# Optimization experiments

Measured on AMD Instinct MI355X. Metric: run time of the kernel, lower is better.

The kernel has to match this reference:

```python
import jax, jax.numpy as jnp
import numpy as np

GRAVITY = 9.81007  # pypose default, gravity vector [0,0,g]

# Quaternions are xyzw (pypose SO3 convention). q1*q2 composes rotations R1@R2.

def qmul(q1, q2):
    v1, w1 = q1[..., :3], q1[..., 3:]
    v2, w2 = q2[..., :3], q2[..., 3:]
    w = w1 * w2 - jnp.sum(v1 * v2, axis=-1, keepdims=True)
    v = w1 * v2 + w2 * v1 + jnp.cross(v1, v2)
    return jnp.concatenate([v, w], axis=-1)

def qinv(q):
    return jnp.concatenate([-q[..., :3], q[..., 3:]], axis=-1)

def qrot(q, v):
    # rotate vector v by unit quaternion q: v + 2*cross(qv, cross(qv,v) + qw*v)
    qv, qw = q[..., :3], q[..., 3:]
    t = jnp.cross(qv, v) + qw * v
    return v + 2.0 * jnp.cross(qv, t)

def so3_exp(phi):
    # so3 -> SO3 quaternion: q = [phi*sin(|phi|/2)/|phi|, cos(|phi|/2)]
    theta = jnp.linalg.norm(phi, axis=-1, keepdims=True)
    small = theta < 1e-6
    safe = jnp.where(small, 1.0, theta)
    k = jnp.where(small, 0.5 - theta * theta / 48.0, jnp.sin(0.5 * theta) / safe)
    return jnp.concatenate([phi * k, jnp.cos(0.5 * theta)], axis=-1)


def setup_inputs() -> dict:
    key = jax.random.key(0)
    ks = jax.random.split(key, 7)
    B, F = 64, 32768
    dt = jax.random.uniform(ks[0], (B, F, 1), jnp.float32) * 0.01 + 0.004
    gyro = jax.random.normal(ks[1], (B, F, 3), jnp.float32) * 0.1
    acc = jax.random.normal(ks[2], (B, F, 3), jnp.float32)

    def rand_quat(k, shape):
        q = jax.random.normal(k, shape + (4,), jnp.float32)
        return q / jnp.linalg.norm(q, axis=-1, keepdims=True)

    gt_rot = rand_quat(ks[3], (B, F))      # ground-truth orientations (xyzw)
    init_rot = rand_quat(ks[4], (B, 1))
    init_vel = jax.random.normal(ks[5], (B, 1, 3), jnp.float32)
    init_pos = jax.random.normal(ks[6], (B, 1, 3), jnp.float32)
    return dict(dt=dt, gyro=gyro, acc=acc, gt_rot=gt_rot,
                init_rot=init_rot, init_vel=init_vel, init_pos=init_pos)


def reference(dt, gyro, acc, gt_rot, init_rot, init_vel, init_pos):
    # IMU preintegration (pypose IMUPreintegrator, reset=True, prop_cov=False,
    # training branch: gravity removed in body frame via ground-truth rot).
    g = jnp.array([0.0, 0.0, GRAVITY], dtype=dt.dtype)
    dr = so3_exp(gyro * dt)                                   # (B,F,4) per-step rotation
    # cumulative rotation increment: incre_r[i] = dr_0 * dr_1 * ... * dr_i
    incre_r = jax.lax.associative_scan(qmul, dr, axis=1)      # (B,F,4)
    # gravity-compensated body-frame acceleration
    a = acc - qrot(qinv(gt_rot), g)                           # (B,F,3)
    ra = qrot(incre_r, a)                                     # rotated into init frame
    incre_v = jnp.cumsum(ra * dt, axis=1)                     # (B,F,3)
    v_prev = jnp.concatenate([jnp.zeros_like(incre_v[:, :1]), incre_v[:, :-1]], axis=1)
    incre_p = jnp.cumsum(v_prev * dt + 0.5 * ra * dt * dt, axis=1)
    incre_t = jnp.cumsum(dt, axis=1)                          # (B,F,1)
    # compose with initial state
    rot = qmul(init_rot, incre_r)                             # (B,F,4)
    vel = init_vel + qrot(init_rot, incre_v)                  # (B,F,3)
    pos = init_pos + init_vel * incre_t + qrot(init_rot, incre_p)  # (B,F,3)
    return rot, vel, pos
```

## Files before the change

### kernel.cpp

```cpp
#include <hip/hip_runtime.h>
#include <math.h>

namespace {

constexpr int SEQ    = 4;
constexpr int WCHUNK = 64 * SEQ;

constexpr int GY_F  = 0;
constexpr int AC_F  = 768;
constexpr int GT_F  = 1536;
constexpr int BUF_F = 2560;

struct V3 { float x, y, z; };
struct Q4 { float x, y, z, w; };
struct St { Q4 q; V3 s; V3 p; float T; float pad; };

__device__ __forceinline__ Q4 qmul(const Q4 a, const Q4 b) {
  Q4 r;
  r.x = a.w*b.x + b.w*a.x + a.y*b.z - a.z*b.y;
  r.y = a.w*b.y + b.w*a.y + a.z*b.x - a.x*b.z;
  r.z = a.w*b.z + b.w*a.z + a.x*b.y - a.y*b.x;
  r.w = a.w*b.w - a.x*b.x - a.y*b.y - a.z*b.z;
  return r;
}

__device__ __forceinline__ V3 qrot(const Q4 q, const V3 v) {
  float tx = q.y*v.z - q.z*v.y + q.w*v.x;
  float ty = q.z*v.x - q.x*v.z + q.w*v.y;
  float tz = q.x*v.y - q.y*v.x + q.w*v.z;
  V3 r;
  r.x = v.x + 2.0f*(q.y*tz - q.z*ty);
  r.y = v.y + 2.0f*(q.z*tx - q.x*tz);
  r.z = v.z + 2.0f*(q.x*ty - q.y*tx);
  return r;
}

__device__ __forceinline__ St combine(const St a, const St b) {
  St r;
  r.q = qmul(a.q, b.q);
  V3 rs = qrot(a.q, b.s);
  r.s.x = a.s.x + rs.x;
  r.s.y = a.s.y + rs.y;
  r.s.z = a.s.z + rs.z;
  V3 rp = qrot(a.q, b.p);
  r.p.x = a.p.x + a.s.x*b.T + rp.x;
  r.p.y = a.p.y + a.s.y*b.T + rp.y;
  r.p.z = a.p.z + a.s.z*b.T + rp.z;
  r.T = a.T + b.T;
  r.pad = 0.0f;
  return r;
}

__device__ __forceinline__ St identity_st() {
  St r;
  r.q = {0.0f, 0.0f, 0.0f, 1.0f};
  r.s = {0.0f, 0.0f, 0.0f};
  r.p = {0.0f, 0.0f, 0.0f};
  r.T = 0.0f; r.pad = 0.0f;
  return r;
}

struct El { Q4 q; V3 s; float dt; };

__device__ __forceinline__ El elem_state(float dt, V3 w, V3 ac, Q4 gt) {
  float px = w.x*dt, py = w.y*dt, pz = w.z*dt;
  float t2 = px*px + py*py + pz*pz;
  float k  = 0.5f + t2*(-1.0f/48.0f  + t2*(1.0f/3840.0f));
  float cw = 1.0f + t2*(-0.125f      + t2*(1.0f/384.0f));
  Q4 dr = { px*k, py*k, pz*k, cw };
  Q4 gi = { -gt.x, -gt.y, -gt.z, gt.w };
  V3 g  = { 0.0f, 0.0f, 9.81007f };
  V3 gr = qrot(gi, g);
  V3 a  = { ac.x - gr.x, ac.y - gr.y, ac.z - gr.z };
  V3 ra = qrot(dr, a);
  El e;
  e.q = dr;
  e.s = { ra.x*dt, ra.y*dt, ra.z*dt };
  e.dt = dt;
  return e;
}

__device__ __forceinline__ Q4 shfl_up_q(const Q4 v, int d) {
  return { __shfl_up(v.x,d), __shfl_up(v.y,d), __shfl_up(v.z,d), __shfl_up(v.w,d) };
}
__device__ __forceinline__ V3 shfl_up_v(const V3 v, int d) {
  return { __shfl_up(v.x,d), __shfl_up(v.y,d), __shfl_up(v.z,d) };
}

__device__ __forceinline__ St shfl_up_st(const St& v, int d) {
  St r;
  r.q.x = __shfl_up(v.q.x, d); r.q.y = __shfl_up(v.q.y, d);
  r.q.z = __shfl_up(v.q.z, d); r.q.w = __shfl_up(v.q.w, d);
  r.s.x = __shfl_up(v.s.x, d); r.s.y = __shfl_up(v.s.y, d);
  r.s.z = __shfl_up(v.s.z, d);
  r.p.x = __shfl_up(v.p.x, d); r.p.y = __shfl_up(v.p.y, d);
  r.p.z = __shfl_up(v.p.z, d);
  r.T   = __shfl_up(v.T, d);   r.pad = 0.0f;
  return r;
}

__device__ __forceinline__ St bcast_st(const St& v, int src) {
  St r;
  r.q.x = __shfl(v.q.x, src); r.q.y = __shfl(v.q.y, src);
  r.q.z = __shfl(v.q.z, src); r.q.w = __shfl(v.q.w, src);
  r.s.x = __shfl(v.s.x, src); r.s.y = __shfl(v.s.y, src);
  r.s.z = __shfl(v.s.z, src);
  r.p.x = __shfl(v.p.x, src); r.p.y = __shfl(v.p.y, src);
  r.p.z = __shfl(v.p.z, src);
  r.T   = __shfl(v.T, src);   r.pad = 0.0f;
  return r;
}

__device__ __forceinline__ int swz(int byteoff) {
  return byteoff ^ (((byteoff >> 8) & 3) << 4);
}
__device__ __forceinline__ float4& L4(float* lds, int fidx) {
  return *reinterpret_cast<float4*>(reinterpret_cast<char*>(lds) + swz(fidx << 2));
}

__device__ __forceinline__ void stage16(const void* gsrc, void* ldst) {
  __builtin_amdgcn_global_load_lds(
      (const __attribute__((address_space(1))) void*)gsrc,
      (__attribute__((address_space(3))) void*)ldst, 16, 0, 0);
}

#define STAGE_REGION(gbase, bufByte, nK)                                       \
  {                                                                            \
    _Pragma("unroll")                                                          \
    for (int k = 0; k < (nK); ++k) {                                           \
      int db = k*1024 + t*16;                                                  \
      const char* src = (const char*)(gbase) + swz(db);                        \
      char* ldst = (char*)lds + (bufByte) + k*1024;                            \
      stage16(src, ldst);                                                      \
    }                                                                          \
  }

struct Compressed { float cq[12]; float cs[12]; float cdt[4]; };
struct Seg { Q4 q; V3 s; V3 p; float T; };
struct ScanRes { Q4 qex, qin; V3 sex, sin; V3 pex, pin; float Tex, Tin; };

__device__ __forceinline__ Seg build_slim(float* lds, int ofs, int t,
                                          float4 dt4, Compressed& C) {
  float gy[12], ac[12], gq[16];
  #pragma unroll
  for (int j = 0; j < 3; ++j) ((float4*)gy)[j] = L4(lds, ofs + GY_F + 12*t + 4*j);
  #pragma unroll
  for (int j = 0; j < 3; ++j) ((float4*)ac)[j] = L4(lds, ofs + AC_F + 12*t + 4*j);
  #pragma unroll
  for (int j = 0; j < 4; ++j) ((float4*)gq)[j] = L4(lds, ofs + GT_F + 16*t + 4*j);
  const float dtv[4] = {dt4.x, dt4.y, dt4.z, dt4.w};
  Seg s;
  #pragma unroll
  for (int i = 0; i < SEQ; ++i) {
    El e = elem_state(dtv[i],
               {gy[3*i], gy[3*i+1], gy[3*i+2]},
               {ac[3*i], ac[3*i+1], ac[3*i+2]},
               {gq[4*i], gq[4*i+1], gq[4*i+2], gq[4*i+3]});
    C.cq[3*i] = e.q.x; C.cq[3*i+1] = e.q.y; C.cq[3*i+2] = e.q.z;
    C.cs[3*i] = e.s.x; C.cs[3*i+1] = e.s.y; C.cs[3*i+2] = e.s.z;
    C.cdt[i]  = e.dt;
    if (i == 0) {
      s.q = e.q; s.s = e.s;
      float h = 0.5f*e.dt;
      s.p = { e.s.x*h, e.s.y*h, e.s.z*h };
      s.T = e.dt;
    } else {
      V3 v = qrot(s.q, e.s);
      float h = 0.5f*e.dt;
      s.p.x += s.s.x*e.dt + v.x*h;
      s.p.y += s.s.y*e.dt + v.y*h;
      s.p.z += s.s.z*e.dt + v.z*h;
      s.s.x += v.x; s.s.y += v.y; s.s.z += v.z;
      s.q = qmul(s.q, e.q);
      s.T += e.dt;
    }
  }
  return s;
}

__device__ __forceinline__ ScanRes wave_split_scan(int t, const Seg& sg) {
  ScanRes r;
  Q4 qin = sg.q;
  #pragma unroll
  for (int d = 1; d < 64; d <<= 1) {
    Q4 o = shfl_up_q(qin, d);
    if (t >= d) qin = qmul(o, qin);
  }
  Q4 qex = shfl_up_q(qin, 1);
  if (t == 0) qex = {0.0f, 0.0f, 0.0f, 1.0f};
  V3 v = qrot(qex, sg.s);
  V3 sin_ = v;
  #pragma unroll
  for (int d = 1; d < 64; d <<= 1) {
    V3 o = shfl_up_v(sin_, d);
    if (t >= d) { sin_.x += o.x; sin_.y += o.y; sin_.z += o.z; }
  }
  V3 sex = shfl_up_v(sin_, 1);
  if (t == 0) sex = {0.0f, 0.0f, 0.0f};
  float Tin = sg.T;
  #pragma unroll
  for (int d = 1; d < 64; d <<= 1) {
    float o = __shfl_up(Tin, d);
    if (t >= d) Tin += o;
  }
  float Tex = __shfl_up(Tin, 1);
  if (t == 0) Tex = 0.0f;
  V3 w = qrot(qex, sg.p);
  V3 u = { w.x + sex.x*sg.T, w.y + sex.y*sg.T, w.z + sex.z*sg.T };
  V3 pin = u;
  #pragma unroll
  for (int d = 1; d < 64; d <<= 1) {
    V3 o = shfl_up_v(pin, d);
    if (t >= d) { pin.x += o.x; pin.y += o.y; pin.z += o.z; }
  }
  V3 pex = shfl_up_v(pin, 1);
  if (t == 0) pex = {0.0f, 0.0f, 0.0f};
  r.qex = qex; r.qin = qin;
  r.sex = sex; r.sin = sin_;
  r.pex = pex; r.pin = pin;
  r.Tex = Tex; r.Tin = Tin;
  return r;
}

__device__ __forceinline__ void compute_outputs(
    const Compressed& C, Q4 Pq, V3 Ps, V3 Pp, float PT,
    const ScanRes& S, V3 iv, V3 ip,
    float* rotb , float* velb , float* posb )
{
  Q4 Xq = qmul(Pq, S.qex);
  V3 rs = qrot(Pq, S.sex);
  V3 Xs = { Ps.x + rs.x, Ps.y + rs.y, Ps.z + rs.z };
  V3 rp = qrot(Pq, S.pex);
  V3 Xp = { Pp.x + Ps.x*S.Tex + rp.x, Pp.y + Ps.y*S.Tex + rp.y,
            Pp.z + Ps.z*S.Tex + rp.z };
  float XT = PT + S.Tex;

  Q4 qr = Xq; V3 sr = Xs; V3 pr = Xp; float Tr = XT;
  #pragma unroll
  for (int i = 0; i < SEQ; ++i) {
    float qx = C.cq[3*i], qy = C.cq[3*i+1], qz = C.cq[3*i+2];
    Q4 eq = { qx, qy, qz, sqrtf(fmaxf(1.0f - qx*qx - qy*qy - qz*qz, 0.0f)) };
    V3 es = { C.cs[3*i], C.cs[3*i+1], C.cs[3*i+2] };
    float dt = C.cdt[i], h = 0.5f*dt;
    V3 vv = qrot(qr, es);
    V3 pn = { pr.x + sr.x*dt + vv.x*h,
              pr.y + sr.y*dt + vv.y*h,
              pr.z + sr.z*dt + vv.z*h };
    V3 sn = { sr.x + vv.x, sr.y + vv.y, sr.z + vv.z };
    Q4 qn = qmul(qr, eq);
    float Tn = Tr + dt;
    rotb[4*i+0] = qn.x; rotb[4*i+1] = qn.y; rotb[4*i+2] = qn.z; rotb[4*i+3] = qn.w;
    velb[3*i+0] = iv.x + sn.x;
    velb[3*i+1] = iv.y + sn.y;
    velb[3*i+2] = iv.z + sn.z;
    posb[3*i+0] = ip.x + iv.x*Tn + pn.x;
    posb[3*i+1] = ip.y + iv.y*Tn + pn.y;
    posb[3*i+2] = ip.z + iv.z*Tn + pn.z;
    qr = qn; sr = sn; pr = pn; Tr = Tn;
  }
}

__global__ __launch_bounds__(64) void k_agg(
    const float* __restrict__ dtp, const float* __restrict__ gyp,
    const float* __restrict__ acp, const float* __restrict__ gtp,
    St* __restrict__ aggs)
{
  __shared__ __align__(16) float lds[BUF_F];
  const int t = threadIdx.x;
  const size_t base = (size_t)blockIdx.x * WCHUNK;

  STAGE_REGION(gyp + base*3, 0,    3);
  STAGE_REGION(acp + base*3, 3072, 3);
  STAGE_REGION(gtp + base*4, 6144, 4);
  float4 dt4 = ((const float4*)(dtp + base))[t];
  __syncthreads();

  Compressed C;
  Seg s = build_slim(lds, 0, t, dt4, C);
  ScanRes R = wave_split_scan(t, s);

  if (t == 63) {
    St a;
    a.q = R.qin; a.s = R.sin; a.p = R.pin; a.T = R.Tin; a.pad = 0.0f;
    aggs[blockIdx.x] = a;
  }
}

__global__ __launch_bounds__(64) void k_pref(
    const St* __restrict__ aggs, const float* __restrict__ irp,
    float* __restrict__ prefb, int cpb)
{
  const int b = blockIdx.x;
  const int lane = threadIdx.x & 63;

  St carry = identity_st();
  carry.q = { irp[b*4+0], irp[b*4+1], irp[b*4+2], irp[b*4+3] };

  const int nw = (cpb + 63) >> 6;
  for (int w = 0; w < nw; ++w) {
    const int idx = (w << 6) + lane;
    St A = identity_st();
    if (idx < cpb) A = aggs[(size_t)b*cpb + idx];
    #pragma unroll
    for (int d = 1; d < 64; d <<= 1) {
      St o = shfl_up_st(A, d);
      if (lane >= d) A = combine(o, A);
    }
    St ex = shfl_up_st(A, 1);
    St P = (lane == 0) ? carry : combine(carry, ex);
    if (idx < cpb) {
      float4* pp = (float4*)(prefb + ((size_t)b*cpb + idx)*12);
      pp[0] = make_float4(P.q.x, P.q.y, P.q.z, P.q.w);
      pp[1] = make_float4(P.s.x, P.s.y, P.s.z, P.p.x);
      pp[2] = make_float4(P.p.y, P.p.z, P.T, 0.0f);
    }
    carry = combine(carry, bcast_st(A, 63));
  }
}

__global__ __launch_bounds__(64) void k_emit(
    const float* __restrict__ dtp, const float* __restrict__ gyp,
    const float* __restrict__ acp, const float* __restrict__ gtp,
    const float* __restrict__ prefb,
    const float* __restrict__ ivp, const float* __restrict__ ipp,
    float* __restrict__ out, int F, int cpb, int B)
{
  __shared__ __align__(16) float lds[2*BUF_F];
  const int t = threadIdx.x;
  const int cid0 = blockIdx.x*2, cid1 = cid0 + 1;
  const int b0 = cid0 / cpb, b1 = cid1 / cpb;
  const size_t base0 = (size_t)cid0 * WCHUNK;
  const size_t base1 = (size_t)cid1 * WCHUNK;

  Q4 Pq0, Pq1; V3 Ps0, Pp0, Ps1, Pp1; float PT0, PT1;
  {
    const float4* pp = (const float4*)(prefb + (size_t)cid0*12);
    float4 a = pp[0], bb = pp[1], cc = pp[2];
    Pq0 = {a.x, a.y, a.z, a.w}; Ps0 = {bb.x, bb.y, bb.z};
    Pp0 = {bb.w, cc.x, cc.y};   PT0 = cc.z;
  }
  {
    const float4* pp = (const float4*)(prefb + (size_t)cid1*12);
    float4 a = pp[0], bb = pp[1], cc = pp[2];
    Pq1 = {a.x, a.y, a.z, a.w}; Ps1 = {bb.x, bb.y, bb.z};
    Pp1 = {bb.w, cc.x, cc.y};   PT1 = cc.z;
  }
  V3 iv0 = { ivp[b0*3+0], ivp[b0*3+1], ivp[b0*3+2] };
  V3 ip0 = { ipp[b0*3+0], ipp[b0*3+1], ipp[b0*3+2] };
  V3 iv1 = { ivp[b1*3+0], ivp[b1*3+1], ivp[b1*3+2] };
  V3 ip1 = { ipp[b1*3+0], ipp[b1*3+1], ipp[b1*3+2] };

  STAGE_REGION(gyp + base0*3, 0,    3);
  STAGE_REGION(acp + base0*3, 3072, 3);
  STAGE_REGION(gtp + base0*4, 6144, 4);
  float4 dt4_0 = ((const float4*)(dtp + base0))[t];
  __syncthreads();

  STAGE_REGION(gyp + base1*3, 10240,      3);
  STAGE_REGION(acp + base1*3, 10240+3072, 3);
  STAGE_REGION(gtp + base1*4, 10240+6144, 4);
  float4 dt4_1 = ((const float4*)(dtp + base1))[t];

  float rotb[16], velb[12], posb[12];
  {
    Compressed C;
    Seg s0 = build_slim(lds, 0, t, dt4_0, C);
    ScanRes R0 = wave_split_scan(t, s0);
    compute_outputs(C, Pq0, Ps0, Pp0, PT0, R0, iv0, ip0, rotb, velb, posb);
  }

  __syncthreads();

  #pragma unroll
  for (int i = 0; i < 4; ++i) L4(lds, GT_F + 4*(4*t + i)) = ((float4*)rotb)[i];
  #pragma unroll
  for (int j = 0; j < 3; ++j) L4(lds, GY_F + 12*t + 4*j) = ((float4*)velb)[j];
  #pragma unroll
  for (int j = 0; j < 3; ++j) L4(lds, AC_F + 12*t + 4*j) = ((float4*)posb)[j];
  __syncthreads();

  const size_t BF = (size_t)B * (size_t)F;
  {
    float4* grot = (float4*)out + base0;
    float4* gvel = (float4*)(out + BF*4 + base0*3);
    float4* gpos = (float4*)(out + BF*7 + base0*3);
    #pragma unroll
    for (int k = 0; k < 4; ++k) grot[t + 64*k] = L4(lds, GT_F + 4*(t + 64*k));
    #pragma unroll
    for (int k = 0; k < 3; ++k) gvel[t + 64*k] = L4(lds, GY_F + 4*(t + 64*k));
    #pragma unroll
    for (int k = 0; k < 3; ++k) gpos[t + 64*k] = L4(lds, AC_F + 4*(t + 64*k));
  }

  {
    Compressed C;
    Seg s1 = build_slim(lds, BUF_F, t, dt4_1, C);
    ScanRes R1 = wave_split_scan(t, s1);
    compute_outputs(C, Pq1, Ps1, Pp1, PT1, R1, iv1, ip1, rotb, velb, posb);
  }

  #pragma unroll
  for (int i = 0; i < 4; ++i) L4(lds, BUF_F + GT_F + 4*(4*t + i)) = ((float4*)rotb)[i];
  #pragma unroll
  for (int j = 0; j < 3; ++j) L4(lds, BUF_F + GY_F + 12*t + 4*j) = ((float4*)velb)[j];
  #pragma unroll
  for (int j = 0; j < 3; ++j) L4(lds, BUF_F + AC_F + 12*t + 4*j) = ((float4*)posb)[j];
  __syncthreads();

  {
    float4* grot = (float4*)out + base1;
    float4* gvel = (float4*)(out + BF*4 + base1*3);
    float4* gpos = (float4*)(out + BF*7 + base1*3);
    #pragma unroll
    for (int k = 0; k < 4; ++k) grot[t + 64*k] = L4(lds, BUF_F + GT_F + 4*(t + 64*k));
    #pragma unroll
    for (int k = 0; k < 3; ++k) gvel[t + 64*k] = L4(lds, BUF_F + GY_F + 4*(t + 64*k));
    #pragma unroll
    for (int k = 0; k < 3; ++k) gpos[t + 64*k] = L4(lds, BUF_F + AC_F + 4*(t + 64*k));
  }
}

}

extern "C" void kernel_launch(void* const* d_in, const int* in_sizes, int n_in,
                              void* d_out, int out_size, void* d_ws, size_t ws_size,
                              hipStream_t stream)
{
  (void)n_in; (void)out_size; (void)ws_size;

  const float* dtp = (const float*)d_in[0];
  const float* gyp = (const float*)d_in[1];
  const float* acp = (const float*)d_in[2];
  const float* gtp = (const float*)d_in[3];
  const float* irp = (const float*)d_in[4];
  const float* ivp = (const float*)d_in[5];
  const float* ipp = (const float*)d_in[6];
  float* out = (float*)d_out;

  const int B   = in_sizes[4] / 4;
  const int F   = in_sizes[0] / B;
  const int cpb = F / WCHUNK;
  const int nchunk = B * cpb;

  St*    aggs  = (St*)d_ws;
  float* prefb = (float*)((char*)d_ws + (size_t)nchunk * sizeof(St));

  k_agg <<<nchunk,   64, 0, stream>>>(dtp, gyp, acp, gtp, aggs);
  k_pref<<<B,        64, 0, stream>>>(aggs, irp, prefb, cpb);
  k_emit<<<nchunk/2, 64, 0, stream>>>(dtp, gyp, acp, gtp, prefb, ivp, ipp,
                                      out, F, cpb, B);
}
```

Baseline: 69.05 us.

## Stage inputs through registers and emit one chunk per block

Replaces the asynchronous global-to-LDS staging with plain float4 loads into registers, followed by swizzled LDS writes. The block-wide barrier after staging is dropped, since each block is a single wave. The emit kernel no longer processes two chunks per block with a double-buffered LDS region; each block now handles one chunk, which doubles the grid and halves LDS use. Launch bounds gain a minimum-occupancy hint. The aim is higher occupancy and simpler staging, at the cost of losing the explicit overlap between the second chunk's loads and the first chunk's compute.

```diff
diff --git a/kernel.cpp b/kernel.cpp
--- a/kernel.cpp
+++ b/kernel.cpp
@@ -9,7 +9,7 @@
 constexpr int GY_F  = 0;
 constexpr int AC_F  = 768;
 constexpr int GT_F  = 1536;
-constexpr int BUF_F = 2560;
+constexpr int LDS_F = 2560;
 
 struct V3 { float x, y, z; };
 struct Q4 { float x, y, z, w; };
@@ -118,36 +118,39 @@
   return *reinterpret_cast<float4*>(reinterpret_cast<char*>(lds) + swz(fidx << 2));
 }
 
-__device__ __forceinline__ void stage16(const void* gsrc, void* ldst) {
-  __builtin_amdgcn_global_load_lds(
-      (const __attribute__((address_space(1))) void*)gsrc,
-      (__attribute__((address_space(3))) void*)ldst, 16, 0, 0);
-}
-
-#define STAGE_REGION(gbase, bufByte, nK)                                       \
-  {                                                                            \
-    _Pragma("unroll")                                                          \
-    for (int k = 0; k < (nK); ++k) {                                           \
-      int db = k*1024 + t*16;                                                  \
-      const char* src = (const char*)(gbase) + swz(db);                        \
-      char* ldst = (char*)lds + (bufByte) + k*1024;                            \
-      stage16(src, ldst);                                                      \
-    }                                                                          \
-  }
-
 struct Compressed { float cq[12]; float cs[12]; float cdt[4]; };
 struct Seg { Q4 q; V3 s; V3 p; float T; };
 struct ScanRes { Q4 qex, qin; V3 sex, sin; V3 pex, pin; float Tex, Tin; };
 
-__device__ __forceinline__ Seg build_slim(float* lds, int ofs, int t,
+__device__ __forceinline__ void reg_stage(float* lds, int t,
+    const float* gyp, const float* acp, const float* gtp, size_t base) {
+  const float4* ggy = (const float4*)(gyp + base*3);
+  const float4* gac = (const float4*)(acp + base*3);
+  const float4* ggt = (const float4*)(gtp + base*4);
+  float4 rgy0 = ggy[t], rgy1 = ggy[t+64], rgy2 = ggy[t+128];
+  float4 rac0 = gac[t], rac1 = gac[t+64], rac2 = gac[t+128];
+  L4(lds, GY_F + 4*t)       = rgy0;
+  L4(lds, GY_F + 4*(t+64))  = rgy1;
+  L4(lds, GY_F + 4*(t+128)) = rgy2;
+  float4 rgt0 = ggt[t], rgt1 = ggt[t+64], rgt2 = ggt[t+128], rgt3 = ggt[t+192];
+  L4(lds, AC_F + 4*t)       = rac0;
+  L4(lds, AC_F + 4*(t+64))  = rac1;
+  L4(lds, AC_F + 4*(t+128)) = rac2;
+  L4(lds, GT_F + 4*t)       = rgt0;
+  L4(lds, GT_F + 4*(t+64))  = rgt1;
+  L4(lds, GT_F + 4*(t+128)) = rgt2;
+  L4(lds, GT_F + 4*(t+192)) = rgt3;
+}
+
+__device__ __forceinline__ Seg build_slim(float* lds, int t,
                                           float4 dt4, Compressed& C) {
   float gy[12], ac[12], gq[16];
   #pragma unroll
-  for (int j = 0; j < 3; ++j) ((float4*)gy)[j] = L4(lds, ofs + GY_F + 12*t + 4*j);
-  #pragma unroll
-  for (int j = 0; j < 3; ++j) ((float4*)ac)[j] = L4(lds, ofs + AC_F + 12*t + 4*j);
-  #pragma unroll
-  for (int j = 0; j < 4; ++j) ((float4*)gq)[j] = L4(lds, ofs + GT_F + 16*t + 4*j);
+  for (int j = 0; j < 3; ++j) ((float4*)gy)[j] = L4(lds, GY_F + 12*t + 4*j);
+  #pragma unroll
+  for (int j = 0; j < 3; ++j) ((float4*)ac)[j] = L4(lds, AC_F + 12*t + 4*j);
+  #pragma unroll
+  for (int j = 0; j < 4; ++j) ((float4*)gq)[j] = L4(lds, GT_F + 16*t + 4*j);
   const float dtv[4] = {dt4.x, dt4.y, dt4.z, dt4.w};
   Seg s;
   #pragma unroll
@@ -222,61 +225,20 @@
   return r;
 }
 
-__device__ __forceinline__ void compute_outputs(
-    const Compressed& C, Q4 Pq, V3 Ps, V3 Pp, float PT,
-    const ScanRes& S, V3 iv, V3 ip,
-    float* rotb , float* velb , float* posb )
-{
-  Q4 Xq = qmul(Pq, S.qex);
-  V3 rs = qrot(Pq, S.sex);
-  V3 Xs = { Ps.x + rs.x, Ps.y + rs.y, Ps.z + rs.z };
-  V3 rp = qrot(Pq, S.pex);
-  V3 Xp = { Pp.x + Ps.x*S.Tex + rp.x, Pp.y + Ps.y*S.Tex + rp.y,
-            Pp.z + Ps.z*S.Tex + rp.z };
-  float XT = PT + S.Tex;
-
-  Q4 qr = Xq; V3 sr = Xs; V3 pr = Xp; float Tr = XT;
-  #pragma unroll
-  for (int i = 0; i < SEQ; ++i) {
-    float qx = C.cq[3*i], qy = C.cq[3*i+1], qz = C.cq[3*i+2];
-    Q4 eq = { qx, qy, qz, sqrtf(fmaxf(1.0f - qx*qx - qy*qy - qz*qz, 0.0f)) };
-    V3 es = { C.cs[3*i], C.cs[3*i+1], C.cs[3*i+2] };
-    float dt = C.cdt[i], h = 0.5f*dt;
-    V3 vv = qrot(qr, es);
-    V3 pn = { pr.x + sr.x*dt + vv.x*h,
-              pr.y + sr.y*dt + vv.y*h,
-              pr.z + sr.z*dt + vv.z*h };
-    V3 sn = { sr.x + vv.x, sr.y + vv.y, sr.z + vv.z };
-    Q4 qn = qmul(qr, eq);
-    float Tn = Tr + dt;
-    rotb[4*i+0] = qn.x; rotb[4*i+1] = qn.y; rotb[4*i+2] = qn.z; rotb[4*i+3] = qn.w;
-    velb[3*i+0] = iv.x + sn.x;
-    velb[3*i+1] = iv.y + sn.y;
-    velb[3*i+2] = iv.z + sn.z;
-    posb[3*i+0] = ip.x + iv.x*Tn + pn.x;
-    posb[3*i+1] = ip.y + iv.y*Tn + pn.y;
-    posb[3*i+2] = ip.z + iv.z*Tn + pn.z;
-    qr = qn; sr = sn; pr = pn; Tr = Tn;
-  }
-}
-
-__global__ __launch_bounds__(64) void k_agg(
+__global__ __launch_bounds__(64, 4) void k_agg(
     const float* __restrict__ dtp, const float* __restrict__ gyp,
     const float* __restrict__ acp, const float* __restrict__ gtp,
     St* __restrict__ aggs)
 {
-  __shared__ __align__(16) float lds[BUF_F];
+  __shared__ __align__(16) float lds[LDS_F];
   const int t = threadIdx.x;
   const size_t base = (size_t)blockIdx.x * WCHUNK;
 
-  STAGE_REGION(gyp + base*3, 0,    3);
-  STAGE_REGION(acp + base*3, 3072, 3);
-  STAGE_REGION(gtp + base*4, 6144, 4);
   float4 dt4 = ((const float4*)(dtp + base))[t];
-  __syncthreads();
+  reg_stage(lds, t, gyp, acp, gtp, base);
 
   Compressed C;
-  Seg s = build_slim(lds, 0, t, dt4, C);
+  Seg s = build_slim(lds, t, dt4, C);
   ScanRes R = wave_split_scan(t, s);
 
   if (t == 63) {
@@ -318,106 +280,90 @@
   }
 }
 
-__global__ __launch_bounds__(64) void k_emit(
+__global__ __launch_bounds__(64, 4) void k_emit(
     const float* __restrict__ dtp, const float* __restrict__ gyp,
     const float* __restrict__ acp, const float* __restrict__ gtp,
     const float* __restrict__ prefb,
     const float* __restrict__ ivp, const float* __restrict__ ipp,
     float* __restrict__ out, int F, int cpb, int B)
 {
-  __shared__ __align__(16) float lds[2*BUF_F];
+  __shared__ __align__(16) float lds[LDS_F];
   const int t = threadIdx.x;
-  const int cid0 = blockIdx.x*2, cid1 = cid0 + 1;
-  const int b0 = cid0 / cpb, b1 = cid1 / cpb;
-  const size_t base0 = (size_t)cid0 * WCHUNK;
-  const size_t base1 = (size_t)cid1 * WCHUNK;
-
-  Q4 Pq0, Pq1; V3 Ps0, Pp0, Ps1, Pp1; float PT0, PT1;
+  const int cid = blockIdx.x;
+  const int b = cid / cpb;
+  const size_t base = (size_t)cid * WCHUNK;
+
+  Q4 Pq; V3 Ps, Pp; float PT;
   {
-    const float4* pp = (const float4*)(prefb + (size_t)cid0*12);
+    const float4* pp = (const float4*)(prefb + (size_t)cid*12);
     float4 a = pp[0], bb = pp[1], cc = pp[2];
-    Pq0 = {a.x, a.y, a.z, a.w}; Ps0 = {bb.x, bb.y, bb.z};
-    Pp0 = {bb.w, cc.x, cc.y};   PT0 = cc.z;
-  }
+    Pq = {a.x, a.y, a.z, a.w};
+    Ps = {bb.x, bb.y, bb.z};
+    Pp = {bb.w, cc.x, cc.y};
+    PT = cc.z;
+  }
+  V3 iv = { ivp[b*3+0], ivp[b*3+1], ivp[b*3+2] };
+  V3 ip = { ipp[b*3+0], ipp[b*3+1], ipp[b*3+2] };
+
+  float4 dt4 = ((const float4*)(dtp + base))[t];
+  reg_stage(lds, t, gyp, acp, gtp, base);
+
+  Compressed C;
+  Seg s = build_slim(lds, t, dt4, C);
+  ScanRes S = wave_split_scan(t, s);
+
+  Q4 Xq = qmul(Pq, S.qex);
+  V3 rs = qrot(Pq, S.sex);
+  V3 Xs = { Ps.x + rs.x, Ps.y + rs.y, Ps.z + rs.z };
+  V3 rp = qrot(Pq, S.pex);
+  V3 Xp = { Pp.x + Ps.x*S.Tex + rp.x, Pp.y + Ps.y*S.Tex + rp.y,
+            Pp.z + Ps.z*S.Tex + rp.z };
+  float XT = PT + S.Tex;
+
+  __syncthreads();
+
   {
-    const float4* pp = (const float4*)(prefb + (size_t)cid1*12);
-    float4 a = pp[0], bb = pp[1], cc = pp[2];
-    Pq1 = {a.x, a.y, a.z, a.w}; Ps1 = {bb.x, bb.y, bb.z};
-    Pp1 = {bb.w, cc.x, cc.y};   PT1 = cc.z;
-  }
-  V3 iv0 = { ivp[b0*3+0], ivp[b0*3+1], ivp[b0*3+2] };
-  V3 ip0 = { ipp[b0*3+0], ipp[b0*3+1], ipp[b0*3+2] };
-  V3 iv1 = { ivp[b1*3+0], ivp[b1*3+1], ivp[b1*3+2] };
-  V3 ip1 = { ipp[b1*3+0], ipp[b1*3+1], ipp[b1*3+2] };
-
-  STAGE_REGION(gyp + base0*3, 0,    3);
-  STAGE_REGION(acp + base0*3, 3072, 3);
-  STAGE_REGION(gtp + base0*4, 6144, 4);
-  float4 dt4_0 = ((const float4*)(dtp + base0))[t];
+    Q4 qr = Xq; V3 sr = Xs; V3 pr = Xp; float Tr = XT;
+    float velb[12], posb[12];
+    #pragma unroll
+    for (int i = 0; i < SEQ; ++i) {
+      float qx = C.cq[3*i], qy = C.cq[3*i+1], qz = C.cq[3*i+2];
+      Q4 eq = { qx, qy, qz, sqrtf(fmaxf(1.0f - qx*qx - qy*qy - qz*qz, 0.0f)) };
+      V3 es = { C.cs[3*i], C.cs[3*i+1], C.cs[3*i+2] };
+      float dt = C.cdt[i], h = 0.5f*dt;
+      V3 vv = qrot(qr, es);
+      V3 pn = { pr.x + sr.x*dt + vv.x*h,
+                pr.y + sr.y*dt + vv.y*h,
+                pr.z + sr.z*dt + vv.z*h };
+      V3 sn = { sr.x + vv.x, sr.y + vv.y, sr.z + vv.z };
+      Q4 qn = qmul(qr, eq);
+      float Tn = Tr + dt;
+      L4(lds, GT_F + 4*(4*t + i)) = make_float4(qn.x, qn.y, qn.z, qn.w);
+      velb[3*i+0] = iv.x + sn.x;
+      velb[3*i+1] = iv.y + sn.y;
+      velb[3*i+2] = iv.z + sn.z;
+      posb[3*i+0] = ip.x + iv.x*Tn + pn.x;
+      posb[3*i+1] = ip.y + iv.y*Tn + pn.y;
+      posb[3*i+2] = ip.z + iv.z*Tn + pn.z;
+      qr = qn; sr = sn; pr = pn; Tr = Tn;
+    }
+    #pragma unroll
+    for (int j = 0; j < 3; ++j) L4(lds, GY_F + 12*t + 4*j) = ((float4*)velb)[j];
+    #pragma unroll
+    for (int j = 0; j < 3; ++j) L4(lds, AC_F + 12*t + 4*j) = ((float4*)posb)[j];
+  }
   __syncthreads();
 
-  STAGE_REGION(gyp + base1*3, 10240,      3);
-  STAGE_REGION(acp + base1*3, 10240+3072, 3);
-  STAGE_REGION(gtp + base1*4, 10240+6144, 4);
-  float4 dt4_1 = ((const float4*)(dtp + base1))[t];
-
-  float rotb[16], velb[12], posb[12];
-  {
-    Compressed C;
-    Seg s0 = build_slim(lds, 0, t, dt4_0, C);
-    ScanRes R0 = wave_split_scan(t, s0);
-    compute_outputs(C, Pq0, Ps0, Pp0, PT0, R0, iv0, ip0, rotb, velb, posb);
-  }
-
-  __syncthreads();
-
-  #pragma unroll
-  for (int i = 0; i < 4; ++i) L4(lds, GT_F + 4*(4*t + i)) = ((float4*)rotb)[i];
-  #pragma unroll
-  for (int j = 0; j < 3; ++j) L4(lds, GY_F + 12*t + 4*j) = ((float4*)velb)[j];
-  #pragma unroll
-  for (int j = 0; j < 3; ++j) L4(lds, AC_F + 12*t + 4*j) = ((float4*)posb)[j];
-  __syncthreads();
-
   const size_t BF = (size_t)B * (size_t)F;
-  {
-    float4* grot = (float4*)out + base0;
-    float4* gvel = (float4*)(out + BF*4 + base0*3);
-    float4* gpos = (float4*)(out + BF*7 + base0*3);
-    #pragma unroll
-    for (int k = 0; k < 4; ++k) grot[t + 64*k] = L4(lds, GT_F + 4*(t + 64*k));
-    #pragma unroll
-    for (int k = 0; k < 3; ++k) gvel[t + 64*k] = L4(lds, GY_F + 4*(t + 64*k));
-    #pragma unroll
-    for (int k = 0; k < 3; ++k) gpos[t + 64*k] = L4(lds, AC_F + 4*(t + 64*k));
-  }
-
-  {
-    Compressed C;
-    Seg s1 = build_slim(lds, BUF_F, t, dt4_1, C);
-    ScanRes R1 = wave_split_scan(t, s1);
-    compute_outputs(C, Pq1, Ps1, Pp1, PT1, R1, iv1, ip1, rotb, velb, posb);
-  }
-
-  #pragma unroll
-  for (int i = 0; i < 4; ++i) L4(lds, BUF_F + GT_F + 4*(4*t + i)) = ((float4*)rotb)[i];
-  #pragma unroll
-  for (int j = 0; j < 3; ++j) L4(lds, BUF_F + GY_F + 12*t + 4*j) = ((float4*)velb)[j];
-  #pragma unroll
-  for (int j = 0; j < 3; ++j) L4(lds, BUF_F + AC_F + 12*t + 4*j) = ((float4*)posb)[j];
-  __syncthreads();
-
-  {
-    float4* grot = (float4*)out + base1;
-    float4* gvel = (float4*)(out + BF*4 + base1*3);
-    float4* gpos = (float4*)(out + BF*7 + base1*3);
-    #pragma unroll
-    for (int k = 0; k < 4; ++k) grot[t + 64*k] = L4(lds, BUF_F + GT_F + 4*(t + 64*k));
-    #pragma unroll
-    for (int k = 0; k < 3; ++k) gvel[t + 64*k] = L4(lds, BUF_F + GY_F + 4*(t + 64*k));
-    #pragma unroll
-    for (int k = 0; k < 3; ++k) gpos[t + 64*k] = L4(lds, BUF_F + AC_F + 4*(t + 64*k));
-  }
+  float4* grot = (float4*)out + base;
+  float4* gvel = (float4*)(out + BF*4 + base*3);
+  float4* gpos = (float4*)(out + BF*7 + base*3);
+  #pragma unroll
+  for (int k = 0; k < 4; ++k) grot[t + 64*k] = L4(lds, GT_F + 4*(t + 64*k));
+  #pragma unroll
+  for (int k = 0; k < 3; ++k) gvel[t + 64*k] = L4(lds, GY_F + 4*(t + 64*k));
+  #pragma unroll
+  for (int k = 0; k < 3; ++k) gpos[t + 64*k] = L4(lds, AC_F + 4*(t + 64*k));
 }
 
 }
@@ -445,8 +391,8 @@
   St*    aggs  = (St*)d_ws;
   float* prefb = (float*)((char*)d_ws + (size_t)nchunk * sizeof(St));
 
-  k_agg <<<nchunk,   64, 0, stream>>>(dtp, gyp, acp, gtp, aggs);
-  k_pref<<<B,        64, 0, stream>>>(aggs, irp, prefb, cpb);
-  k_emit<<<nchunk/2, 64, 0, stream>>>(dtp, gyp, acp, gtp, prefb, ivp, ipp,
-                                      out, F, cpb, B);
-}
+  k_agg <<<nchunk, 64, 0, stream>>>(dtp, gyp, acp, gtp, aggs);
+  k_pref<<<B,      64, 0, stream>>>(aggs, irp, prefb, cpb);
+  k_emit<<<nchunk, 64, 0, stream>>>(dtp, gyp, acp, gtp, prefb, ivp, ipp,
+                                    out, F, cpb, B);
+}
```

New measurement: 79.71 us. 1.15x slower.
